# Kernel tuning notes

Hardware: AMD Instinct MI355X
Metric: run time of the kernel (lower is better)

The kernel has to match this reference:

```python
import jax, jax.numpy as jnp
import numpy as np

HIDDEN = 2048
N_HEADS = 16
N_KV_HEADS = 4
HEAD_DIM = HIDDEN // N_HEADS  # 128
ROPE_THETA = 10000.0
BATCH = 2
SEQ = 2048


def setup_inputs() -> dict:
    key = jax.random.key(0)
    k1, k2, k3, k4, k5 = jax.random.split(key, 5)
    s = 0.02
    return {
        "hidden_states": jax.random.normal(k1, (BATCH, SEQ, HIDDEN), dtype=jnp.float32),
        "attention_mask": jnp.zeros((BATCH, 1, 1, SEQ), dtype=jnp.float32),
        "Wq": jax.random.normal(k2, (HIDDEN, N_HEADS * HEAD_DIM), dtype=jnp.float32) * s,
        "Wk": jax.random.normal(k3, (HIDDEN, N_KV_HEADS * HEAD_DIM), dtype=jnp.float32) * s,
        "Wv": jax.random.normal(k4, (HIDDEN, N_KV_HEADS * HEAD_DIM), dtype=jnp.float32) * s,
        "Wo": jax.random.normal(k5, (N_HEADS * HEAD_DIM, HIDDEN), dtype=jnp.float32) * s,
    }


def _rope_cos_sin(seq_len, dtype):
    inv_freq = 1.0 / (ROPE_THETA ** (jnp.arange(0, HEAD_DIM, 2, dtype=jnp.float32) / HEAD_DIM))
    t = jnp.arange(seq_len, dtype=jnp.float32)
    freqs = t[:, None] * inv_freq[None, :]            # [S, D/2]
    emb = jnp.concatenate([freqs, freqs], axis=-1)    # [S, D]
    cos = jnp.cos(emb)[None, None, :, :].astype(dtype)  # [1,1,S,D]
    sin = jnp.sin(emb)[None, None, :, :].astype(dtype)
    return cos, sin


def _apply_rope(x, cos, sin):
    # x: [B,H,S,D]; faithful to torch code: rotated = cat((-x[...,1::2], x[...,::2]), -1)
    x1 = x[..., ::2]
    x2 = x[..., 1::2]
    rotated = jnp.concatenate([-x2, x1], axis=-1)
    return x * cos + rotated * sin


def reference(hidden_states, attention_mask, Wq, Wk, Wv, Wo):
    B, S, _ = hidden_states.shape
    scale = HEAD_DIM ** -0.5

    q = (hidden_states @ Wq).reshape(B, S, N_HEADS, HEAD_DIM).transpose(0, 2, 1, 3)      # [B,H,S,D]
    k = (hidden_states @ Wk).reshape(B, S, N_KV_HEADS, HEAD_DIM).transpose(0, 2, 1, 3)   # [B,KV,S,D]
    v = (hidden_states @ Wv).reshape(B, S, N_KV_HEADS, HEAD_DIM).transpose(0, 2, 1, 3)

    cos, sin = _rope_cos_sin(S, hidden_states.dtype)
    q = _apply_rope(q, cos, sin)
    k = _apply_rope(k, cos, sin)

    rep = N_HEADS // N_KV_HEADS
    k = jnp.repeat(k, rep, axis=1)  # [B,H,S,D]
    v = jnp.repeat(v, rep, axis=1)

    scores = jnp.einsum("bhqd,bhkd->bhqk", q, k) * scale  # [B,H,S,S]
    causal = jnp.tril(jnp.ones((S, S), dtype=bool))[None, None]
    scores = jnp.where(causal, scores, -jnp.inf)
    scores = scores + attention_mask  # additive float mask, broadcast [B,1,1,S]

    attn = jax.nn.softmax(scores, axis=-1)
    out = jnp.einsum("bhqk,bhkd->bhqd", attn, v)           # [B,H,S,D]
    out = out.transpose(0, 2, 1, 3).reshape(B, S, N_HEADS * HEAD_DIM)
    return out @ Wo
```

## Files before the change

kernel.cpp:

```cpp
#include <hip/hip_runtime.h>
#include <hip/hip_bf16.h>

#define BATCH 2
#define SEQ   2048
#define NH    16
#define NKV   4
#define HD    128
#define KDIM  2048
#define MROWS 4096
#define NQKV  3072

typedef __attribute__((ext_vector_type(8))) short  s16x8;
typedef __attribute__((ext_vector_type(4))) short  s16x4;
typedef __attribute__((ext_vector_type(4))) float  f32x4;
typedef __attribute__((ext_vector_type(8))) __bf16 b16x8;

#define BARRIER_LDS() do { \
    asm volatile("s_waitcnt lgkmcnt(0)" ::: "memory"); \
    __builtin_amdgcn_s_barrier(); \
  } while (0)

__device__ __forceinline__ unsigned short f2bf(float f) {
  __hip_bfloat16 h = __float2bfloat16(f);
  return *reinterpret_cast<unsigned short*>(&h);
}
__device__ __forceinline__ float bf2f(unsigned short h) {
  union { unsigned int u; float f; } x; x.u = ((unsigned int)h) << 16;
  return x.f;
}

__device__ __forceinline__ f32x4 MFMA16(s16x8 a, s16x8 b, f32x4 c) {
  return __builtin_amdgcn_mfma_f32_16x16x32_bf16(
      __builtin_bit_cast(b16x8, a), __builtin_bit_cast(b16x8, b), c, 0, 0, 0);
}

__device__ __forceinline__ void gload_lds16(const void* g, void* lds) {
  __builtin_amdgcn_global_load_lds(
      (const __attribute__((address_space(1))) void*)g,
      (__attribute__((address_space(3))) void*)lds, 16, 0, 0);
}

__global__ __launch_bounds__(256) void prep_weights(
    const float* __restrict__ Wq, const float* __restrict__ Wk,
    const float* __restrict__ Wv, const float* __restrict__ Wo,
    unsigned short* __restrict__ BT, unsigned short* __restrict__ WoT) {
  __shared__ float tile[32][33];
  int bx = blockIdx.x;
  const float* W; unsigned short* WT; int Nd, nb;
  if (bx < 64)       { W = Wq; WT = BT;                          Nd = 2048; nb = bx; }
  else if (bx < 80)  { W = Wk; WT = BT + (size_t)2048 * KDIM;    Nd = 512;  nb = bx - 64; }
  else if (bx < 96)  { W = Wv; WT = BT + (size_t)2560 * KDIM;    Nd = 512;  nb = bx - 80; }
  else               { W = Wo; WT = WoT;                         Nd = 2048; nb = bx - 96; }
  int n0 = nb * 32, k0 = blockIdx.y * 32;
  int tx = threadIdx.x & 31, ty = threadIdx.x >> 5;
#pragma unroll
  for (int i = 0; i < 4; ++i)
    tile[ty + i * 8][tx] = W[(size_t)(k0 + ty + i * 8) * Nd + n0 + tx];
  __syncthreads();
#pragma unroll
  for (int i = 0; i < 4; ++i)
    WT[(size_t)(n0 + ty + i * 8) * KDIM + k0 + tx] = f2bf(tile[tx][ty + i * 8]);
}

__global__ __launch_bounds__(256) void conv_bf16(
    const float* __restrict__ X, unsigned short* __restrict__ Y) {
  int i = blockIdx.x * 256 + threadIdx.x;
  const float4 a = ((const float4*)X)[2 * i];
  const float4 b = ((const float4*)X)[2 * i + 1];
  s16x8 o;
  o[0] = (short)f2bf(a.x); o[1] = (short)f2bf(a.y);
  o[2] = (short)f2bf(a.z); o[3] = (short)f2bf(a.w);
  o[4] = (short)f2bf(b.x); o[5] = (short)f2bf(b.y);
  o[6] = (short)f2bf(b.z); o[7] = (short)f2bf(b.w);
  ((s16x8*)Y)[i] = o;
}

__global__ __launch_bounds__(256) void rope_table_kernel(float* __restrict__ tbl) {
  int i = blockIdx.x * 256 + threadIdx.x;
  int s = i >> 6, j = i & 63;
  float inv = powf(10000.0f, -(float)(2 * j) * (1.0f / 128.0f));
  float f = (float)s * inv;
  tbl[2 * i]     = cosf(f);
  tbl[2 * i + 1] = sinf(f);
}

__global__ __launch_bounds__(256) void gemm_qkv(
    const unsigned short* __restrict__ A, const unsigned short* __restrict__ BT,
    unsigned short* __restrict__ Qo, unsigned short* __restrict__ Ko,
    unsigned short* __restrict__ Vo) {
  __shared__ __align__(16) unsigned short la[128][32];
  __shared__ __align__(16) unsigned short lb[128][32];
  int tid = threadIdx.x, lane = tid & 63, w = tid >> 6;
  int lin = blockIdx.x;
  int swz = (lin & 7) * 96 + (lin >> 3);
  int bx = swz % 24, by = swz / 24;
  int m0 = by * 128, n0 = bx * 128;
  int wr = (w >> 1) * 64, wc = (w & 1) * 64;
  int fr = lane & 15, kg = (lane >> 4) * 8, rg = (lane >> 4) * 4;
  f32x4 acc[4][4] = {};
  for (int kt = 0; kt < KDIM; kt += 32) {
    __syncthreads();
#pragma unroll
    for (int i = 0; i < 2; ++i) {
      int idx = tid + i * 256;
      int row = idx >> 2, seg = idx & 3;
      gload_lds16(A + (size_t)(m0 + row) * KDIM + kt + seg * 8,
                  (char*)la + (size_t)(i * 256 + w * 64) * 16);
      gload_lds16(BT + (size_t)(n0 + row) * KDIM + kt + seg * 8,
                  (char*)lb + (size_t)(i * 256 + w * 64) * 16);
    }
    __syncthreads();
    s16x8 af[4], bf[4];
#pragma unroll
    for (int mi = 0; mi < 4; ++mi) af[mi] = *(const s16x8*)(&la[wr + mi * 16 + fr][kg]);
#pragma unroll
    for (int ni = 0; ni < 4; ++ni) bf[ni] = *(const s16x8*)(&lb[wc + ni * 16 + fr][kg]);
#pragma unroll
    for (int mi = 0; mi < 4; ++mi)
#pragma unroll
      for (int ni = 0; ni < 4; ++ni) acc[mi][ni] = MFMA16(af[mi], bf[ni], acc[mi][ni]);
  }
  int rbase = m0 + wr + rg;
#pragma unroll
  for (int ni = 0; ni < 4; ++ni) {
    int gn = n0 + wc + ni * 16 + fr;
    if (gn < 2048) {
      int hh = gn >> 7, d = gn & 127;
#pragma unroll
      for (int mi = 0; mi < 4; ++mi)
#pragma unroll
        for (int r = 0; r < 4; ++r) {
          int grow = rbase + mi * 16 + r;
          int bb = grow >> 11, ss = grow & 2047;
          Qo[((size_t)(bb * NH + hh) * SEQ + ss) * HD + d] = f2bf(acc[mi][ni][r]);
        }
    } else if (gn < 2560) {
      int c = gn - 2048, kvh = c >> 7, d = c & 127;
#pragma unroll
      for (int mi = 0; mi < 4; ++mi)
#pragma unroll
        for (int r = 0; r < 4; ++r) {
          int grow = rbase + mi * 16 + r;
          int bb = grow >> 11, ss = grow & 2047;
          Ko[((size_t)(bb * NKV + kvh) * SEQ + ss) * HD + d] = f2bf(acc[mi][ni][r]);
        }
    } else {
      int c = gn - 2560, kvh = c >> 7, d = c & 127;
#pragma unroll
      for (int mi = 0; mi < 4; ++mi) {
        int grow0 = rbase + mi * 16;
        int bb = grow0 >> 11, ss = grow0 & 2047;
        s16x4 pk;
#pragma unroll
        for (int r = 0; r < 4; ++r) pk[r] = (short)f2bf(acc[mi][ni][r]);
        *(s16x4*)(Vo + ((size_t)(bb * NKV + kvh) * HD + d) * SEQ + ss) = pk;
      }
    }
  }
}

__global__ __launch_bounds__(256) void gemm_out(
    const unsigned short* __restrict__ A, const unsigned short* __restrict__ BT,
    float* __restrict__ C) {
  __shared__ __align__(16) unsigned short la[128][32];
  __shared__ __align__(16) unsigned short lb[128][32];
  int tid = threadIdx.x, lane = tid & 63, w = tid >> 6;
  int lin = blockIdx.x;
  int swz = (lin & 7) * 64 + (lin >> 3);
  int bx = swz % 16, by = swz / 16;
  int m0 = by * 128, n0 = bx * 128;
  int wr = (w >> 1) * 64, wc = (w & 1) * 64;
  int fr = lane & 15, kg = (lane >> 4) * 8, rg = (lane >> 4) * 4;
  f32x4 acc[4][4] = {};
  for (int kt = 0; kt < KDIM; kt += 32) {
    __syncthreads();
#pragma unroll
    for (int i = 0; i < 2; ++i) {
      int idx = tid + i * 256;
      int row = idx >> 2, seg = idx & 3;
      gload_lds16(A + (size_t)(m0 + row) * KDIM + kt + seg * 8,
                  (char*)la + (size_t)(i * 256 + w * 64) * 16);
      gload_lds16(BT + (size_t)(n0 + row) * KDIM + kt + seg * 8,
                  (char*)lb + (size_t)(i * 256 + w * 64) * 16);
    }
    __syncthreads();
    s16x8 af[4], bf[4];
#pragma unroll
    for (int mi = 0; mi < 4; ++mi) af[mi] = *(const s16x8*)(&la[wr + mi * 16 + fr][kg]);
#pragma unroll
    for (int ni = 0; ni < 4; ++ni) bf[ni] = *(const s16x8*)(&lb[wc + ni * 16 + fr][kg]);
#pragma unroll
    for (int mi = 0; mi < 4; ++mi)
#pragma unroll
      for (int ni = 0; ni < 4; ++ni) acc[mi][ni] = MFMA16(af[mi], bf[ni], acc[mi][ni]);
  }
  int rbase = m0 + wr + rg;
#pragma unroll
  for (int ni = 0; ni < 4; ++ni) {
    int gn = n0 + wc + ni * 16 + fr;
#pragma unroll
    for (int mi = 0; mi < 4; ++mi)
#pragma unroll
      for (int r = 0; r < 4; ++r)
        C[(size_t)(rbase + mi * 16 + r) * 2048 + gn] = acc[mi][ni][r];
  }
}

__global__ __launch_bounds__(256) void rope2(
    unsigned short* __restrict__ Qx, unsigned short* __restrict__ Kx,
    const float* __restrict__ tbl) {
  __shared__ __align__(16) unsigned short xs[32][136];
  int tid = threadIdx.x;
  int bid = blockIdx.x;
  unsigned short* X;
  size_t r0;
  if (bid < 2048) { X = Qx; r0 = (size_t)bid * 32; }
  else            { X = Kx; r0 = (size_t)(bid - 2048) * 32; }
#pragma unroll
  for (int i = 0; i < 2; ++i) {
    int idx = tid + i * 256;
    int pr = idx >> 4, seg = idx & 15;
    *(s16x8*)(&xs[pr][seg * 8]) = *(const s16x8*)(X + (r0 + pr) * 128 + seg * 8);
  }
  __syncthreads();
  int pr = tid >> 3, jb = (tid & 7) * 8;
  size_t row = r0 + pr;
  int s = (int)(row & (SEQ - 1));
  s16x8 o0, o1;
#pragma unroll
  for (int j0 = 0; j0 < 8; ++j0) {
    int j = jb + j0;
    float c  = tbl[(s * 64 + j) * 2];
    float sn = tbl[(s * 64 + j) * 2 + 1];
    float xj   = bf2f(xs[pr][j]);
    float xj64 = bf2f(xs[pr][j + 64]);
    float x2j  = bf2f(xs[pr][2 * j]);
    float x2j1 = bf2f(xs[pr][2 * j + 1]);
    o0[j0] = (short)f2bf(xj * c - x2j1 * sn);
    o1[j0] = (short)f2bf(xj64 * c + x2j * sn);
  }
  unsigned short* xp = X + row * 128;
  *(s16x8*)(xp + jb)      = o0;
  *(s16x8*)(xp + 64 + jb) = o1;
}

__global__ __launch_bounds__(256, 2) void attn_fwd(
    const unsigned short* __restrict__ Q, const unsigned short* __restrict__ K,
    const unsigned short* __restrict__ VT, const float* __restrict__ mask,
    unsigned short* __restrict__ O) {
  __shared__ __align__(16) unsigned short kt_[2][64][136];
  __shared__ __align__(16) unsigned short vt_[2][128][68];
  __shared__ __align__(16) unsigned short pt_[4][16][36];

  int tid = threadIdx.x, lane = tid & 63, w = tid >> 6;
  int l = blockIdx.x;
  int grp = l & 7, slot = l >> 3;
  int hloc = slot & 3, qt = 31 - (slot >> 2);
  int b = grp >> 2, kvh = grp & 3, h = kvh * 4 + hloc;
  int qbase = qt * 64;
  int qw = qbase + w * 16;
  int fr = lane & 15, g = lane >> 4, kg = g * 8, rg = g * 4;

  const unsigned short* Qb = Q + (size_t)(b * NH + h) * SEQ * HD;
  const unsigned short* Kb = K + (size_t)(b * NKV + kvh) * SEQ * HD;
  const unsigned short* Vb = VT + (size_t)(b * NKV + kvh) * HD * SEQ;
  const float* mb = mask + (size_t)b * SEQ;

  int krow = tid >> 4, kpos = (tid & 15) * 8;
  int vrow0 = tid >> 3, vcol = (tid & 7) * 8;
  const float sc2 = 0.12751744584812722f;
  const float L2E = 1.44269504088896f;
  int bS = b * SEQ;
  int ntiles = qt + 1;

  s16x8 aq[4];
#pragma unroll
  for (int dc = 0; dc < 4; ++dc)
    aq[dc] = *(const s16x8*)(Qb + (size_t)(qw + fr) * HD + dc * 32 + kg);

  f32x4 oacc[8] = {};
  float m_r = -3e38f, l_r = 0.f;

  s16x8 kreg[4], vreg[4];
#pragma unroll
  for (int i = 0; i < 4; ++i)
    kreg[i] = *(const s16x8*)(Kb + (size_t)(krow + i * 16) * HD + kpos);
#pragma unroll
  for (int i = 0; i < 4; ++i) {
    int c = tid + 256 * i;
    vreg[i] = *(const s16x8*)(Vb + (size_t)(c >> 3) * SEQ + (c & 7) * 8);
  }
#pragma unroll
  for (int i = 0; i < 4; ++i)
    *(s16x8*)(&kt_[0][krow + i * 16][kpos]) = kreg[i];
#pragma unroll
  for (int i = 0; i < 4; ++i) {
    int c = tid + 256 * i;
    *(s16x8*)(&vt_[0][c >> 3][(c & 7) * 8]) = vreg[i];
  }
  if (ntiles > 1) {
#pragma unroll
    for (int i = 0; i < 4; ++i)
      kreg[i] = *(const s16x8*)(Kb + (size_t)(64 + krow + i * 16) * HD + kpos);
#pragma unroll
    for (int i = 0; i < 4; ++i) {
      int c = tid + 256 * i;
      vreg[i] = *(const s16x8*)(Vb + (size_t)(c >> 3) * SEQ + 64 + (c & 7) * 8);
    }
  }
  BARRIER_LDS();

  for (int t = 0; t < ntiles; ++t) {
    int kv0 = t * 64;
    int cur = t & 1;
    bool diag = (t == qt);

    if (t + 1 < ntiles) {
#pragma unroll
      for (int i = 0; i < 4; ++i)
        *(s16x8*)(&kt_[cur ^ 1][krow + i * 16][kpos]) = kreg[i];
#pragma unroll
      for (int i = 0; i < 4; ++i) {
        int c = tid + 256 * i;
        *(s16x8*)(&vt_[cur ^ 1][c >> 3][(c & 7) * 8]) = vreg[i];
      }
      if (t + 2 < ntiles) {
#pragma unroll
        for (int i = 0; i < 4; ++i)
          kreg[i] = *(const s16x8*)(Kb + (size_t)(kv0 + 128 + krow + i * 16) * HD + kpos);
#pragma unroll
        for (int i = 0; i < 4; ++i) {
          int c = tid + 256 * i;
          vreg[i] = *(const s16x8*)(Vb + (size_t)(c >> 3) * SEQ + kv0 + 128 + (c & 7) * 8);
        }
      }
    }

    f32x4 sf[4];
    __builtin_amdgcn_s_setprio(1);
#pragma unroll
    for (int mk = 0; mk < 4; ++mk) {
      s16x8 ak[4];
#pragma unroll
      for (int dc = 0; dc < 4; ++dc)
        ak[dc] = *(const s16x8*)(&kt_[cur][mk * 16 + fr][dc * 32 + kg]);
      sf[mk] = f32x4{0.f, 0.f, 0.f, 0.f};
#pragma unroll
      for (int dc = 0; dc < 4; ++dc)
        sf[mk] = MFMA16(ak[dc], aq[dc], sf[mk]);
    }
    __builtin_amdgcn_s_setprio(0);

#pragma unroll
    for (int mk = 0; mk < 4; ++mk) {
      float4 mv = *(const float4*)(mb + kv0 + mk * 16 + rg);
      float mvr[4] = {mv.x * L2E, mv.y * L2E, mv.z * L2E, mv.w * L2E};
      if (diag) {
#pragma unroll
        for (int r = 0; r < 4; ++r) {
          int kv = kv0 + mk * 16 + rg + r;
          float v = sf[mk][r] * sc2 + mvr[r];
          sf[mk][r] = (kv <= qw + fr) ? v : -3e38f;
        }
      } else {
#pragma unroll
        for (int r = 0; r < 4; ++r)
          sf[mk][r] = sf[mk][r] * sc2 + mvr[r];
      }
    }

    float pm01a = fmaxf(sf[0][0], sf[0][1]), pm01b = fmaxf(sf[0][2], sf[0][3]);
    float pm11a = fmaxf(sf[1][0], sf[1][1]), pm11b = fmaxf(sf[1][2], sf[1][3]);
    float pm21a = fmaxf(sf[2][0], sf[2][1]), pm21b = fmaxf(sf[2][2], sf[2][3]);
    float pm31a = fmaxf(sf[3][0], sf[3][1]), pm31b = fmaxf(sf[3][2], sf[3][3]);
    float pm0 = fmaxf(pm01a, pm01b), pm1 = fmaxf(pm11a, pm11b);
    float pm2 = fmaxf(pm21a, pm21b), pm3 = fmaxf(pm31a, pm31b);
    float pm = fmaxf(fmaxf(pm0, pm1), fmaxf(pm2, pm3));
    pm = fmaxf(pm, __shfl_xor(pm, 16, 64));
    pm = fmaxf(pm, __shfl_xor(pm, 32, 64));
    if (!__all(pm - m_r <= 8.0f)) {
      float mo = m_r;
      float mn = fmaxf(mo, pm);
      float al = exp2f(mo - mn);
      m_r = mn;
      l_r *= al;
#pragma unroll
      for (int r = 0; r < 4; ++r) {
        float ar = __shfl(al, rg + r, 16);
#pragma unroll
        for (int od = 0; od < 8; ++od) oacc[od][r] *= ar;
      }
    }
    float rs = 0.f;
#pragma unroll
    for (int mk = 0; mk < 4; ++mk)
#pragma unroll
      for (int r = 0; r < 4; ++r) {
        float ppv = exp2f(sf[mk][r] - m_r);
        sf[mk][r] = ppv;
        rs += ppv;
      }
    rs += __shfl_xor(rs, 16, 64);
    rs += __shfl_xor(rs, 32, 64);
    l_r += rs;

#pragma unroll
    for (int kk = 0; kk < 2; ++kk) {
#pragma unroll
      for (int mh = 0; mh < 2; ++mh) {
        int mk = kk * 2 + mh;
        s16x4 pk;
#pragma unroll
        for (int r = 0; r < 4; ++r) pk[r] = (short)f2bf(sf[mk][r]);
        *(s16x4*)(&pt_[w][fr][mh * 16 + rg]) = pk;
      }
      s16x8 ap = *(const s16x8*)(&pt_[w][fr][kg]);
      __builtin_amdgcn_s_setprio(1);
#pragma unroll
      for (int od = 0; od < 8; ++od) {
        s16x8 bv = *(const s16x8*)(&vt_[cur][od * 16 + fr][kk * 32 + kg]);
        oacc[od] = MFMA16(ap, bv, oacc[od]);
      }
      __builtin_amdgcn_s_setprio(0);
    }

    BARRIER_LDS();
  }

  float iv = 1.0f / l_r;
  float ivr[4];
#pragma unroll
  for (int r = 0; r < 4; ++r) ivr[r] = __shfl(iv, rg + r, 16);
#pragma unroll
  for (int r = 0; r < 4; ++r) {
    unsigned short* op = O + (size_t)(bS + qw + rg + r) * 2048 + h * 128 + fr;
#pragma unroll
    for (int od = 0; od < 8; ++od)
      op[od * 16] = f2bf(oacc[od][r] * ivr[r]);
  }
}

extern "C" void kernel_launch(void* const* d_in, const int* in_sizes, int n_in,
                              void* d_out, int out_size, void* d_ws, size_t ws_size,
                              hipStream_t stream) {
  const float* hidden = (const float*)d_in[0];
  const float* mask   = (const float*)d_in[1];
  const float* Wq     = (const float*)d_in[2];
  const float* Wk     = (const float*)d_in[3];
  const float* Wv     = (const float*)d_in[4];
  const float* Wo     = (const float*)d_in[5];
  float* out = (float*)d_out;

  char* ws = (char*)d_ws;
  unsigned short* BT  = (unsigned short*)(ws);
  unsigned short* WoT = (unsigned short*)(ws + 12582912);
  unsigned short* Qb  = (unsigned short*)(ws + 20971520);
  unsigned short* Kb  = (unsigned short*)(ws + 37748736);
  unsigned short* VT  = (unsigned short*)(ws + 41943040);
  unsigned short* AO  = (unsigned short*)(ws + 46137344);
  float*          tbl = (float*)(ws + 62914560);
  unsigned short* Ab  = AO;

  conv_bf16<<<MROWS * KDIM / (256 * 8), 256, 0, stream>>>(hidden, Ab);
  prep_weights<<<dim3(160, 64), 256, 0, stream>>>(Wq, Wk, Wv, Wo, BT, WoT);
  rope_table_kernel<<<512, 256, 0, stream>>>(tbl);

  gemm_qkv<<<dim3(768), 256, 0, stream>>>(Ab, BT, Qb, Kb, VT);
  rope2<<<dim3(2048 + 512), 256, 0, stream>>>(Qb, Kb, tbl);
  attn_fwd<<<dim3(1024), 256, 0, stream>>>(Qb, Kb, VT, mask, AO);
  gemm_out<<<dim3(512), 256, 0, stream>>>(AO, WoT, out);
}
```

Before: 228.4 us.

## Rewrite attention with 32x32 MFMA, register-resident P, and balanced tile order

The attention kernel now uses 32x32x16 bf16 MFMA with 2 waves per block, each handling 32 query rows. The score tile is converted to the PV operand in registers with cvt_pk_bf16 and permlane32_swap, which removes the LDS round-trip for P and the cross-lane shuffles for row stats. K/V LDS buffering becomes single-buffered with loads interleaved around barriers. Query tiles are ordered to interleave long and short causal tiles for load balance. Less LDS double buffering may expose more memory latency.

```diff
diff --git a/kernel.cpp b/kernel.cpp
--- a/kernel.cpp
+++ b/kernel.cpp
@@ -13,6 +13,7 @@
 typedef __attribute__((ext_vector_type(8))) short  s16x8;
 typedef __attribute__((ext_vector_type(4))) short  s16x4;
 typedef __attribute__((ext_vector_type(4))) float  f32x4;
+typedef __attribute__((ext_vector_type(16))) float f32x16;
 typedef __attribute__((ext_vector_type(8))) __bf16 b16x8;
 
 #define BARRIER_LDS() do { \
@@ -32,6 +33,19 @@
 __device__ __forceinline__ f32x4 MFMA16(s16x8 a, s16x8 b, f32x4 c) {
   return __builtin_amdgcn_mfma_f32_16x16x32_bf16(
       __builtin_bit_cast(b16x8, a), __builtin_bit_cast(b16x8, b), c, 0, 0, 0);
+}
+__device__ __forceinline__ f32x16 MFMA32(s16x8 a, s16x8 b, f32x16 c) {
+  return __builtin_amdgcn_mfma_f32_32x32x16_bf16(
+      __builtin_bit_cast(b16x8, a), __builtin_bit_cast(b16x8, b), c, 0, 0, 0);
+}
+
+__device__ __forceinline__ unsigned cvtpk(float lo, float hi) {
+  unsigned r;
+  asm("v_cvt_pk_bf16_f32 %0, %1, %2" : "=v"(r) : "v"(lo), "v"(hi));
+  return r;
+}
+__device__ __forceinline__ void pl32swap(unsigned &d, unsigned &s) {
+  asm("v_permlane32_swap_b32 %0, %1" : "+v"(d), "+v"(s));
 }
 
 __device__ __forceinline__ void gload_lds16(const void* g, void* lds) {
@@ -244,22 +258,23 @@
   *(s16x8*)(xp + 64 + jb) = o1;
 }
 
-__global__ __launch_bounds__(256, 2) void attn_fwd(
+__global__ __launch_bounds__(128, 2) void attn_fwd(
     const unsigned short* __restrict__ Q, const unsigned short* __restrict__ K,
     const unsigned short* __restrict__ VT, const float* __restrict__ mask,
     unsigned short* __restrict__ O) {
-  __shared__ __align__(16) unsigned short kt_[2][64][136];
-  __shared__ __align__(16) unsigned short vt_[2][128][68];
-  __shared__ __align__(16) unsigned short pt_[4][16][36];
+  __shared__ __align__(16) unsigned short kt_[64][136];
+  __shared__ __align__(16) unsigned short vt_[128][68];
 
   int tid = threadIdx.x, lane = tid & 63, w = tid >> 6;
   int l = blockIdx.x;
   int grp = l & 7, slot = l >> 3;
-  int hloc = slot & 3, qt = 31 - (slot >> 2);
+  int hloc = slot & 3;
+  int sq = slot >> 2, g8 = sq >> 3, pos = sq & 7;
+  int qt = (g8 == 0) ? 31 - pos : (g8 == 1) ? pos : (g8 == 2) ? 23 - pos : 8 + pos;
   int b = grp >> 2, kvh = grp & 3, h = kvh * 4 + hloc;
   int qbase = qt * 64;
-  int qw = qbase + w * 16;
-  int fr = lane & 15, g = lane >> 4, kg = g * 8, rg = g * 4;
+  int qw = qbase + w * 32;
+  int lq = lane & 31, hi = lane >> 5, hi8 = hi * 8;
 
   const unsigned short* Qb = Q + (size_t)(b * NH + h) * SEQ * HD;
   const unsigned short* Kb = K + (size_t)(b * NKV + kvh) * SEQ * HD;
@@ -267,176 +282,161 @@
   const float* mb = mask + (size_t)b * SEQ;
 
   int krow = tid >> 4, kpos = (tid & 15) * 8;
-  int vrow0 = tid >> 3, vcol = (tid & 7) * 8;
   const float sc2 = 0.12751744584812722f;
   const float L2E = 1.44269504088896f;
   int bS = b * SEQ;
   int ntiles = qt + 1;
-
-  s16x8 aq[4];
-#pragma unroll
-  for (int dc = 0; dc < 4; ++dc)
-    aq[dc] = *(const s16x8*)(Qb + (size_t)(qw + fr) * HD + dc * 32 + kg);
-
-  f32x4 oacc[8] = {};
+  int q = qw + lq;
+
+  s16x8 aq[8];
+#pragma unroll
+  for (int st = 0; st < 8; ++st)
+    aq[st] = *(const s16x8*)(Qb + (size_t)q * HD + st * 16 + hi8);
+
+  f32x16 oacc[4] = {};
   float m_r = -3e38f, l_r = 0.f;
 
-  s16x8 kreg[4], vreg[4];
-#pragma unroll
-  for (int i = 0; i < 4; ++i)
-    kreg[i] = *(const s16x8*)(Kb + (size_t)(krow + i * 16) * HD + kpos);
-#pragma unroll
-  for (int i = 0; i < 4; ++i) {
-    int c = tid + 256 * i;
+  s16x8 kreg[8], vreg[8];
+#pragma unroll
+  for (int i = 0; i < 8; ++i)
+    kreg[i] = *(const s16x8*)(Kb + (size_t)(krow + 8 * i) * HD + kpos);
+#pragma unroll
+  for (int i = 0; i < 8; ++i) {
+    int c = tid + 128 * i;
     vreg[i] = *(const s16x8*)(Vb + (size_t)(c >> 3) * SEQ + (c & 7) * 8);
   }
 #pragma unroll
-  for (int i = 0; i < 4; ++i)
-    *(s16x8*)(&kt_[0][krow + i * 16][kpos]) = kreg[i];
-#pragma unroll
-  for (int i = 0; i < 4; ++i) {
-    int c = tid + 256 * i;
-    *(s16x8*)(&vt_[0][c >> 3][(c & 7) * 8]) = vreg[i];
-  }
-  if (ntiles > 1) {
-#pragma unroll
-    for (int i = 0; i < 4; ++i)
-      kreg[i] = *(const s16x8*)(Kb + (size_t)(64 + krow + i * 16) * HD + kpos);
-#pragma unroll
-    for (int i = 0; i < 4; ++i) {
-      int c = tid + 256 * i;
-      vreg[i] = *(const s16x8*)(Vb + (size_t)(c >> 3) * SEQ + 64 + (c & 7) * 8);
-    }
-  }
+  for (int i = 0; i < 8; ++i)
+    *(s16x8*)(&kt_[krow + 8 * i][kpos]) = kreg[i];
   BARRIER_LDS();
 
   for (int t = 0; t < ntiles; ++t) {
     int kv0 = t * 64;
-    int cur = t & 1;
+    bool notlast = (t + 1 < ntiles);
     bool diag = (t == qt);
 
-    if (t + 1 < ntiles) {
-#pragma unroll
-      for (int i = 0; i < 4; ++i)
-        *(s16x8*)(&kt_[cur ^ 1][krow + i * 16][kpos]) = kreg[i];
-#pragma unroll
-      for (int i = 0; i < 4; ++i) {
-        int c = tid + 256 * i;
-        *(s16x8*)(&vt_[cur ^ 1][c >> 3][(c & 7) * 8]) = vreg[i];
-      }
-      if (t + 2 < ntiles) {
-#pragma unroll
-        for (int i = 0; i < 4; ++i)
-          kreg[i] = *(const s16x8*)(Kb + (size_t)(kv0 + 128 + krow + i * 16) * HD + kpos);
-#pragma unroll
-        for (int i = 0; i < 4; ++i) {
-          int c = tid + 256 * i;
-          vreg[i] = *(const s16x8*)(Vb + (size_t)(c >> 3) * SEQ + kv0 + 128 + (c & 7) * 8);
+#pragma unroll
+    for (int i = 0; i < 8; ++i) {
+      int c = tid + 128 * i;
+      *(s16x8*)(&vt_[c >> 3][(c & 7) * 8]) = vreg[i];
+    }
+    if (notlast) {
+#pragma unroll
+      for (int i = 0; i < 8; ++i)
+        kreg[i] = *(const s16x8*)(Kb + (size_t)(kv0 + 64 + krow + 8 * i) * HD + kpos);
+    }
+
+    f32x16 sA = {}, sB = {};
+    __builtin_amdgcn_s_setprio(1);
+#pragma unroll
+    for (int st = 0; st < 8; ++st) {
+      s16x8 ka = *(const s16x8*)(&kt_[lq][st * 16 + hi8]);
+      s16x8 kb = *(const s16x8*)(&kt_[32 + lq][st * 16 + hi8]);
+      sA = MFMA32(ka, aq[st], sA);
+      sB = MFMA32(kb, aq[st], sB);
+    }
+    __builtin_amdgcn_s_setprio(0);
+
+#pragma unroll
+    for (int blk = 0; blk < 2; ++blk) {
+#pragma unroll
+      for (int rq = 0; rq < 4; ++rq) {
+        float4 mv = *(const float4*)(mb + kv0 + blk * 32 + rq * 8 + 4 * hi);
+        float mvr[4] = {mv.x * L2E, mv.y * L2E, mv.z * L2E, mv.w * L2E};
+#pragma unroll
+        for (int j = 0; j < 4; ++j) {
+          int r = rq * 4 + j;
+          float v = (blk ? sB[r] : sA[r]) * sc2 + mvr[j];
+          if (diag) {
+            int kv = kv0 + blk * 32 + rq * 8 + 4 * hi + j;
+            v = (kv <= q) ? v : -3e38f;
+          }
+          if (blk) sB[r] = v; else sA[r] = v;
         }
       }
     }
 
-    f32x4 sf[4];
-    __builtin_amdgcn_s_setprio(1);
-#pragma unroll
-    for (int mk = 0; mk < 4; ++mk) {
-      s16x8 ak[4];
-#pragma unroll
-      for (int dc = 0; dc < 4; ++dc)
-        ak[dc] = *(const s16x8*)(&kt_[cur][mk * 16 + fr][dc * 32 + kg]);
-      sf[mk] = f32x4{0.f, 0.f, 0.f, 0.f};
-#pragma unroll
-      for (int dc = 0; dc < 4; ++dc)
-        sf[mk] = MFMA16(ak[dc], aq[dc], sf[mk]);
-    }
-    __builtin_amdgcn_s_setprio(0);
-
-#pragma unroll
-    for (int mk = 0; mk < 4; ++mk) {
-      float4 mv = *(const float4*)(mb + kv0 + mk * 16 + rg);
-      float mvr[4] = {mv.x * L2E, mv.y * L2E, mv.z * L2E, mv.w * L2E};
-      if (diag) {
-#pragma unroll
-        for (int r = 0; r < 4; ++r) {
-          int kv = kv0 + mk * 16 + rg + r;
-          float v = sf[mk][r] * sc2 + mvr[r];
-          sf[mk][r] = (kv <= qw + fr) ? v : -3e38f;
-        }
-      } else {
-#pragma unroll
-        for (int r = 0; r < 4; ++r)
-          sf[mk][r] = sf[mk][r] * sc2 + mvr[r];
-      }
-    }
-
-    float pm01a = fmaxf(sf[0][0], sf[0][1]), pm01b = fmaxf(sf[0][2], sf[0][3]);
-    float pm11a = fmaxf(sf[1][0], sf[1][1]), pm11b = fmaxf(sf[1][2], sf[1][3]);
-    float pm21a = fmaxf(sf[2][0], sf[2][1]), pm21b = fmaxf(sf[2][2], sf[2][3]);
-    float pm31a = fmaxf(sf[3][0], sf[3][1]), pm31b = fmaxf(sf[3][2], sf[3][3]);
-    float pm0 = fmaxf(pm01a, pm01b), pm1 = fmaxf(pm11a, pm11b);
-    float pm2 = fmaxf(pm21a, pm21b), pm3 = fmaxf(pm31a, pm31b);
-    float pm = fmaxf(fmaxf(pm0, pm1), fmaxf(pm2, pm3));
-    pm = fmaxf(pm, __shfl_xor(pm, 16, 64));
+    float pm = -3e38f;
+#pragma unroll
+    for (int r = 0; r < 16; ++r) pm = fmaxf(pm, fmaxf(sA[r], sB[r]));
     pm = fmaxf(pm, __shfl_xor(pm, 32, 64));
     if (!__all(pm - m_r <= 8.0f)) {
-      float mo = m_r;
-      float mn = fmaxf(mo, pm);
-      float al = exp2f(mo - mn);
+      float mn = fmaxf(m_r, pm);
+      float al = exp2f(m_r - mn);
       m_r = mn;
       l_r *= al;
 #pragma unroll
-      for (int r = 0; r < 4; ++r) {
-        float ar = __shfl(al, rg + r, 16);
-#pragma unroll
-        for (int od = 0; od < 8; ++od) oacc[od][r] *= ar;
-      }
+      for (int d4 = 0; d4 < 4; ++d4)
+#pragma unroll
+        for (int r = 0; r < 16; ++r) oacc[d4][r] *= al;
     }
     float rs = 0.f;
 #pragma unroll
-    for (int mk = 0; mk < 4; ++mk)
-#pragma unroll
-      for (int r = 0; r < 4; ++r) {
-        float ppv = exp2f(sf[mk][r] - m_r);
-        sf[mk][r] = ppv;
-        rs += ppv;
-      }
-    rs += __shfl_xor(rs, 16, 64);
+    for (int r = 0; r < 16; ++r) {
+      float pa = exp2f(sA[r] - m_r), pb = exp2f(sB[r] - m_r);
+      sA[r] = pa; sB[r] = pb;
+      rs += pa + pb;
+    }
     rs += __shfl_xor(rs, 32, 64);
     l_r += rs;
 
-#pragma unroll
-    for (int kk = 0; kk < 2; ++kk) {
-#pragma unroll
-      for (int mh = 0; mh < 2; ++mh) {
-        int mk = kk * 2 + mh;
-        s16x4 pk;
-#pragma unroll
-        for (int r = 0; r < 4; ++r) pk[r] = (short)f2bf(sf[mk][r]);
-        *(s16x4*)(&pt_[w][fr][mh * 16 + rg]) = pk;
+    s16x8 pf[4];
+#pragma unroll
+    for (int ks = 0; ks < 4; ++ks) {
+      int a = (ks & 1) * 8;
+      unsigned X0, X1, Y0, Y1;
+      if (ks < 2) {
+        X0 = cvtpk(sA[a + 0], sA[a + 1]); X1 = cvtpk(sA[a + 2], sA[a + 3]);
+        Y0 = cvtpk(sA[a + 4], sA[a + 5]); Y1 = cvtpk(sA[a + 6], sA[a + 7]);
+      } else {
+        X0 = cvtpk(sB[a + 0], sB[a + 1]); X1 = cvtpk(sB[a + 2], sB[a + 3]);
+        Y0 = cvtpk(sB[a + 4], sB[a + 5]); Y1 = cvtpk(sB[a + 6], sB[a + 7]);
       }
-      s16x8 ap = *(const s16x8*)(&pt_[w][fr][kg]);
-      __builtin_amdgcn_s_setprio(1);
-#pragma unroll
-      for (int od = 0; od < 8; ++od) {
-        s16x8 bv = *(const s16x8*)(&vt_[cur][od * 16 + fr][kk * 32 + kg]);
-        oacc[od] = MFMA16(ap, bv, oacc[od]);
+      pl32swap(X0, Y0);
+      pl32swap(X1, Y1);
+      union { unsigned u[4]; s16x8 v; } pk;
+      pk.u[0] = X0; pk.u[1] = X1; pk.u[2] = Y0; pk.u[3] = Y1;
+      pf[ks] = pk.v;
+    }
+
+    BARRIER_LDS();
+
+    if (notlast) {
+#pragma unroll
+      for (int i = 0; i < 8; ++i)
+        *(s16x8*)(&kt_[krow + 8 * i][kpos]) = kreg[i];
+#pragma unroll
+      for (int i = 0; i < 8; ++i) {
+        int c = tid + 128 * i;
+        vreg[i] = *(const s16x8*)(Vb + (size_t)(c >> 3) * SEQ + kv0 + 64 + (c & 7) * 8);
       }
-      __builtin_amdgcn_s_setprio(0);
-    }
+    }
+
+    __builtin_amdgcn_s_setprio(1);
+#pragma unroll
+    for (int d4 = 0; d4 < 4; ++d4) {
+#pragma unroll
+      for (int ks = 0; ks < 4; ++ks) {
+        s16x8 vf = *(const s16x8*)(&vt_[d4 * 32 + lq][ks * 16 + hi8]);
+        oacc[d4] = MFMA32(vf, pf[ks], oacc[d4]);
+      }
+    }
+    __builtin_amdgcn_s_setprio(0);
 
     BARRIER_LDS();
   }
 
   float iv = 1.0f / l_r;
-  float ivr[4];
-#pragma unroll
-  for (int r = 0; r < 4; ++r) ivr[r] = __shfl(iv, rg + r, 16);
-#pragma unroll
-  for (int r = 0; r < 4; ++r) {
-    unsigned short* op = O + (size_t)(bS + qw + rg + r) * 2048 + h * 128 + fr;
-#pragma unroll
-    for (int od = 0; od < 8; ++od)
-      op[od * 16] = f2bf(oacc[od][r] * ivr[r]);
+  unsigned short* orow = O + (size_t)(bS + q) * 2048 + h * 128;
+#pragma unroll
+  for (int d4 = 0; d4 < 4; ++d4) {
+#pragma unroll
+    for (int rq = 0; rq < 4; ++rq) {
+      s16x4 pk;
+#pragma unroll
+      for (int j = 0; j < 4; ++j) pk[j] = (short)f2bf(oacc[d4][rq * 4 + j] * iv);
+      *(s16x4*)(orow + d4 * 32 + rq * 8 + 4 * hi) = pk;
+    }
   }
 }
 
@@ -467,6 +467,6 @@
 
   gemm_qkv<<<dim3(768), 256, 0, stream>>>(Ab, BT, Qb, Kb, VT);
   rope2<<<dim3(2048 + 512), 256, 0, stream>>>(Qb, Kb, tbl);
-  attn_fwd<<<dim3(1024), 256, 0, stream>>>(Qb, Kb, VT, mask, AO);
+  attn_fwd<<<dim3(1024), 128, 0, stream>>>(Qb, Kb, VT, mask, AO);
   gemm_out<<<dim3(512), 256, 0, stream>>>(AO, WoT, out);
 }
```

Result: slower. 244.8 us (+7.2%).

## Rewrite QKV GEMM with 256x256 tiles, 4-stage LDS pipeline and swizzle

Applied to the files above, without the earlier changes.

The QKV projection GEMM now uses 512-thread blocks computing 256x256 tiles, giving 192 blocks instead of 768. Global-to-LDS loads run through a 4-buffer ring with a prefetch distance of 2 and a vmcnt-based wait, replacing the two __syncthreads per k-step. LDS chunks are XOR-swizzled to cut bank conflicts, and s_setprio is raised around the MFMA bursts. The aim is more data reuse per block and loads overlapped with compute, at the cost of 64 KB LDS per block and fewer blocks than the 256 CUs.

```diff
diff --git a/kernel.cpp b/kernel.cpp
--- a/kernel.cpp
+++ b/kernel.cpp
@@ -84,75 +84,123 @@
   tbl[2 * i + 1] = sinf(f);
 }
 
-__global__ __launch_bounds__(256) void gemm_qkv(
+__global__ __launch_bounds__(512, 2) void gemm_qkv(
     const unsigned short* __restrict__ A, const unsigned short* __restrict__ BT,
     unsigned short* __restrict__ Qo, unsigned short* __restrict__ Ko,
     unsigned short* __restrict__ Vo) {
-  __shared__ __align__(16) unsigned short la[128][32];
-  __shared__ __align__(16) unsigned short lb[128][32];
-  int tid = threadIdx.x, lane = tid & 63, w = tid >> 6;
+  __shared__ __align__(16) unsigned short lds[4][2][8192];
+  int tid = threadIdx.x, lane = tid & 63;
+  int w = tid >> 6, wm = w >> 2, wn = w & 3;
   int lin = blockIdx.x;
-  int swz = (lin & 7) * 96 + (lin >> 3);
-  int bx = swz % 24, by = swz / 24;
-  int m0 = by * 128, n0 = bx * 128;
-  int wr = (w >> 1) * 64, wc = (w & 1) * 64;
-  int fr = lane & 15, kg = (lane >> 4) * 8, rg = (lane >> 4) * 4;
-  f32x4 acc[4][4] = {};
-  for (int kt = 0; kt < KDIM; kt += 32) {
-    __syncthreads();
-#pragma unroll
-    for (int i = 0; i < 2; ++i) {
-      int idx = tid + i * 256;
-      int row = idx >> 2, seg = idx & 3;
-      gload_lds16(A + (size_t)(m0 + row) * KDIM + kt + seg * 8,
-                  (char*)la + (size_t)(i * 256 + w * 64) * 16);
-      gload_lds16(BT + (size_t)(n0 + row) * KDIM + kt + seg * 8,
-                  (char*)lb + (size_t)(i * 256 + w * 64) * 16);
-    }
-    __syncthreads();
-    s16x8 af[4], bf[4];
-#pragma unroll
-    for (int mi = 0; mi < 4; ++mi) af[mi] = *(const s16x8*)(&la[wr + mi * 16 + fr][kg]);
-#pragma unroll
-    for (int ni = 0; ni < 4; ++ni) bf[ni] = *(const s16x8*)(&lb[wc + ni * 16 + fr][kg]);
-#pragma unroll
-    for (int mi = 0; mi < 4; ++mi)
-#pragma unroll
-      for (int ni = 0; ni < 4; ++ni) acc[mi][ni] = MFMA16(af[mi], bf[ni], acc[mi][ni]);
-  }
-  int rbase = m0 + wr + rg;
-#pragma unroll
-  for (int ni = 0; ni < 4; ++ni) {
-    int gn = n0 + wc + ni * 16 + fr;
+  int swz = (lin & 7) * 24 + (lin >> 3);
+  int bx = swz % 12, by = swz / 12;
+  int m0 = by * 256, n0 = bx * 256;
+  int fr = lane & 15, cg4 = lane >> 4, rg4 = (lane >> 4) * 4;
+
+  int rS1 = tid >> 2,        cS1 = (tid & 3) ^ (rS1 & 3);
+  int t2  = tid + 512;
+  int rS2 = t2 >> 2,         cS2 = (t2 & 3) ^ (rS2 & 3);
+
+  f32x4 acc[8][4] = {};
+
+#pragma unroll
+  for (int kt = 0; kt < 2; ++kt) {
+    gload_lds16(A + (size_t)(m0 + rS1) * KDIM + kt * 32 + cS1 * 8,
+                (char*)&lds[kt][0][0] + (size_t)tid * 16);
+    gload_lds16(A + (size_t)(m0 + rS2) * KDIM + kt * 32 + cS2 * 8,
+                (char*)&lds[kt][0][0] + (size_t)t2 * 16);
+    gload_lds16(BT + (size_t)(n0 + rS1) * KDIM + kt * 32 + cS1 * 8,
+                (char*)&lds[kt][1][0] + (size_t)tid * 16);
+    gload_lds16(BT + (size_t)(n0 + rS2) * KDIM + kt * 32 + cS2 * 8,
+                (char*)&lds[kt][1][0] + (size_t)t2 * 16);
+  }
+
+  for (int kt = 0; kt < KDIM / 32; ++kt) {
+    int buf = kt & 3;
+    asm volatile("s_waitcnt vmcnt(4)" ::: "memory");
+    __builtin_amdgcn_s_barrier();
+
+    const unsigned short* lA = &lds[buf][0][0];
+    const unsigned short* lB = &lds[buf][1][0];
+    s16x8 bfr[4], afr[4];
+#pragma unroll
+    for (int nf = 0; nf < 4; ++nf) {
+      int rb = wn * 64 + nf * 16 + fr;
+      bfr[nf] = *(const s16x8*)(lB + rb * 32 + (cg4 ^ (rb & 3)) * 8);
+    }
+#pragma unroll
+    for (int mf = 0; mf < 4; ++mf) {
+      int ra = wm * 128 + mf * 16 + fr;
+      afr[mf] = *(const s16x8*)(lA + ra * 32 + (cg4 ^ (ra & 3)) * 8);
+    }
+    if (kt + 2 < KDIM / 32) {
+      int nb = (kt + 2) & 3, ko = (kt + 2) * 32;
+      gload_lds16(A + (size_t)(m0 + rS1) * KDIM + ko + cS1 * 8,
+                  (char*)&lds[nb][0][0] + (size_t)tid * 16);
+      gload_lds16(A + (size_t)(m0 + rS2) * KDIM + ko + cS2 * 8,
+                  (char*)&lds[nb][0][0] + (size_t)t2 * 16);
+    }
+    __builtin_amdgcn_s_setprio(1);
+#pragma unroll
+    for (int mf = 0; mf < 4; ++mf)
+#pragma unroll
+      for (int nf = 0; nf < 4; ++nf)
+        acc[mf][nf] = MFMA16(afr[mf], bfr[nf], acc[mf][nf]);
+    __builtin_amdgcn_s_setprio(0);
+#pragma unroll
+    for (int mf = 0; mf < 4; ++mf) {
+      int ra = wm * 128 + (mf + 4) * 16 + fr;
+      afr[mf] = *(const s16x8*)(lA + ra * 32 + (cg4 ^ (ra & 3)) * 8);
+    }
+    if (kt + 2 < KDIM / 32) {
+      int nb = (kt + 2) & 3, ko = (kt + 2) * 32;
+      gload_lds16(BT + (size_t)(n0 + rS1) * KDIM + ko + cS1 * 8,
+                  (char*)&lds[nb][1][0] + (size_t)tid * 16);
+      gload_lds16(BT + (size_t)(n0 + rS2) * KDIM + ko + cS2 * 8,
+                  (char*)&lds[nb][1][0] + (size_t)t2 * 16);
+    }
+    __builtin_amdgcn_s_setprio(1);
+#pragma unroll
+    for (int mf = 0; mf < 4; ++mf)
+#pragma unroll
+      for (int nf = 0; nf < 4; ++nf)
+        acc[mf + 4][nf] = MFMA16(afr[mf], bfr[nf], acc[mf + 4][nf]);
+    __builtin_amdgcn_s_setprio(0);
+  }
+
+  int rbase = m0 + wm * 128 + rg4;
+#pragma unroll
+  for (int nf = 0; nf < 4; ++nf) {
+    int gn = n0 + wn * 64 + nf * 16 + fr;
     if (gn < 2048) {
       int hh = gn >> 7, d = gn & 127;
 #pragma unroll
-      for (int mi = 0; mi < 4; ++mi)
+      for (int mf = 0; mf < 8; ++mf)
 #pragma unroll
         for (int r = 0; r < 4; ++r) {
-          int grow = rbase + mi * 16 + r;
+          int grow = rbase + mf * 16 + r;
           int bb = grow >> 11, ss = grow & 2047;
-          Qo[((size_t)(bb * NH + hh) * SEQ + ss) * HD + d] = f2bf(acc[mi][ni][r]);
+          Qo[((size_t)(bb * NH + hh) * SEQ + ss) * HD + d] = f2bf(acc[mf][nf][r]);
         }
     } else if (gn < 2560) {
       int c = gn - 2048, kvh = c >> 7, d = c & 127;
 #pragma unroll
-      for (int mi = 0; mi < 4; ++mi)
+      for (int mf = 0; mf < 8; ++mf)
 #pragma unroll
         for (int r = 0; r < 4; ++r) {
-          int grow = rbase + mi * 16 + r;
+          int grow = rbase + mf * 16 + r;
           int bb = grow >> 11, ss = grow & 2047;
-          Ko[((size_t)(bb * NKV + kvh) * SEQ + ss) * HD + d] = f2bf(acc[mi][ni][r]);
+          Ko[((size_t)(bb * NKV + kvh) * SEQ + ss) * HD + d] = f2bf(acc[mf][nf][r]);
         }
     } else {
       int c = gn - 2560, kvh = c >> 7, d = c & 127;
 #pragma unroll
-      for (int mi = 0; mi < 4; ++mi) {
-        int grow0 = rbase + mi * 16;
+      for (int mf = 0; mf < 8; ++mf) {
+        int grow0 = rbase + mf * 16;
         int bb = grow0 >> 11, ss = grow0 & 2047;
         s16x4 pk;
 #pragma unroll
-        for (int r = 0; r < 4; ++r) pk[r] = (short)f2bf(acc[mi][ni][r]);
+        for (int r = 0; r < 4; ++r) pk[r] = (short)f2bf(acc[mf][nf][r]);
         *(s16x4*)(Vo + ((size_t)(bb * NKV + kvh) * HD + d) * SEQ + ss) = pk;
       }
     }
@@ -267,7 +315,6 @@
   const float* mb = mask + (size_t)b * SEQ;
 
   int krow = tid >> 4, kpos = (tid & 15) * 8;
-  int vrow0 = tid >> 3, vcol = (tid & 7) * 8;
   const float sc2 = 0.12751744584812722f;
   const float L2E = 1.44269504088896f;
   int bS = b * SEQ;
@@ -465,7 +512,7 @@
   prep_weights<<<dim3(160, 64), 256, 0, stream>>>(Wq, Wk, Wv, Wo, BT, WoT);
   rope_table_kernel<<<512, 256, 0, stream>>>(tbl);
 
-  gemm_qkv<<<dim3(768), 256, 0, stream>>>(Ab, BT, Qb, Kb, VT);
+  gemm_qkv<<<dim3(192), 512, 0, stream>>>(Ab, BT, Qb, Kb, VT);
   rope2<<<dim3(2048 + 512), 256, 0, stream>>>(Qb, Kb, tbl);
   attn_fwd<<<dim3(1024), 256, 0, stream>>>(Qb, Kb, VT, mask, AO);
   gemm_out<<<dim3(512), 256, 0, stream>>>(AO, WoT, out);
```

After: 223.0 us. -2.4%, faster.
